# Kernel optimization log

Measured on AMD Instinct MI355X. Metric: run time of the kernel, lower is better.

The kernel has to match this reference:

```python
import jax, jax.numpy as jnp
import numpy as np

NUM_HEADS = 16
EMBD_DIM = 1024


def setup_inputs() -> dict:
    key = jax.random.key(0)
    k_x, k_q, k_k, k_v, k_o = jax.random.split(key, 5)
    BS, SL, ED = 4, 2048, EMBD_DIM
    scale = 1.0 / np.sqrt(ED)
    return {
        "x": jax.random.normal(k_x, (BS, SL, ED), dtype=jnp.float32),
        "Wq": jax.random.normal(k_q, (ED, ED), dtype=jnp.float32) * scale,
        "Wk": jax.random.normal(k_k, (ED, ED), dtype=jnp.float32) * scale,
        "Wv": jax.random.normal(k_v, (ED, ED), dtype=jnp.float32) * scale,
        "Wo": jax.random.normal(k_o, (ED, ED), dtype=jnp.float32) * scale,
    }


def reference(x, Wq, Wk, Wv, Wo):
    BS, SL, ED = x.shape
    NH = NUM_HEADS
    HS = ED // NH
    # QKV projections (no bias), split heads -> [B, H, S, Hs]
    q = (x @ Wq).reshape(BS, SL, NH, HS).transpose(0, 2, 1, 3)
    k = (x @ Wk).reshape(BS, SL, NH, HS).transpose(0, 2, 1, 3)
    v = (x @ Wv).reshape(BS, SL, NH, HS).transpose(0, 2, 1, 3)
    # scaled dot-product scores [B, H, S, S]
    scores = jnp.einsum("bhqd,bhkd->bhqk", q, k) / jnp.sqrt(jnp.float32(HS))
    causal = jnp.tril(jnp.ones((SL, SL), dtype=bool))
    scores = jnp.where(causal, scores, jnp.float32(-jnp.inf))
    attn = jax.nn.softmax(scores, axis=-1)
    # attn_dropout with p=0.0 is identity (eval mode)
    out = jnp.einsum("bhqk,bhkd->bhqd", attn, v)
    out = out.transpose(0, 2, 1, 3).reshape(BS, SL, ED)
    # output projection; resid_dropout p=0.0 is identity
    return out @ Wo
```

## Files before the change

kernel.cpp:

```cpp
#include <hip/hip_runtime.h>

typedef unsigned short u16;
typedef unsigned int u32;
typedef __bf16 bf16x8 __attribute__((ext_vector_type(8)));
typedef float f32x4 __attribute__((ext_vector_type(4)));

__device__ __forceinline__ u16 f2bf(float f) {
  union { float f; u32 u; } v; v.f = f;
  u32 r = v.u + 0x7FFFu + ((v.u >> 16) & 1u);
  return (u16)(r >> 16);
}
__device__ __forceinline__ u32 pk2(float a, float b) {
  return (u32)f2bf(a) | ((u32)f2bf(b) << 16);
}

typedef __attribute__((address_space(1))) const void* gvp;
typedef __attribute__((address_space(3))) void* lvp;
__device__ __forceinline__ void gl16(const u16* g, u16* l) {
  __builtin_amdgcn_global_load_lds((gvp)g, (lvp)l, 16, 0, 0);
}

__global__ void probe_kernel(const u16* __restrict__ x, int* __restrict__ mode) {
  if (threadIdx.x == 0 && blockIdx.x == 0) {
    int cnt = 0;
    for (int i = 0; i < 512; ++i) {
      int e = (x[i] >> 7) & 0xFF;
      cnt += (e >= 110 && e <= 134) ? 1 : 0;
    }
    *mode = (cnt >= 410) ? 1 : 0;
  }
}

__global__ __launch_bounds__(256) void cast_x(const void* __restrict__ src,
                                              u16* __restrict__ dst, int n,
                                              const int* __restrict__ mode) {
  int i = (blockIdx.x * 256 + threadIdx.x) * 8;
  if (i >= n) return;
  uint4 out;
  if (*mode == 0) {
    const float* s = (const float*)src + i;
    float4 v0 = *(const float4*)s, v1 = *(const float4*)(s + 4);
    out.x = pk2(v0.x, v0.y); out.y = pk2(v0.z, v0.w);
    out.z = pk2(v1.x, v1.y); out.w = pk2(v1.z, v1.w);
  } else {
    out = *(const uint4*)((const u16*)src + i);
  }
  *(uint4*)(dst + i) = out;
}

__global__ __launch_bounds__(256) void tcast(const void* __restrict__ src,
                                             u16* __restrict__ dst, int srcld,
                                             int dstld, const int* __restrict__ mode) {
  __shared__ __align__(16) u16 T[64 * 72];
  int k0 = blockIdx.x * 64, n0 = blockIdx.y * 64;
  int tid = threadIdx.x;
  bool bf = (*mode != 0);
#pragma unroll
  for (int p = 0; p < 2; ++p) {
    int idx = (tid + p * 256) * 8;
    int r = idx >> 6, c = idx & 63;
    uint4 o;
    if (!bf) {
      const float* s = (const float*)src + (size_t)(k0 + r) * srcld + n0 + c;
      float4 v0 = *(const float4*)s, v1 = *(const float4*)(s + 4);
      o.x = pk2(v0.x, v0.y); o.y = pk2(v0.z, v0.w);
      o.z = pk2(v1.x, v1.y); o.w = pk2(v1.z, v1.w);
    } else {
      o = *(const uint4*)((const u16*)src + (size_t)(k0 + r) * srcld + n0 + c);
    }
    *(uint4*)&T[r * 72 + c] = o;
  }
  __syncthreads();
#pragma unroll
  for (int p = 0; p < 2; ++p) {
    int idx = (tid + p * 256) * 8;
    int n = idx >> 6, kk = idx & 63;
    u16 v[8];
#pragma unroll
    for (int j = 0; j < 8; ++j) v[j] = T[(kk + j) * 72 + n];
    *(uint4*)(dst + (size_t)(n0 + n) * dstld + k0 + kk) = *(uint4*)v;
  }
}

template<int OUTM>
__global__ __launch_bounds__(256) void gemm_m97(
    const u16* __restrict__ A, const u16* __restrict__ Bt,
    u16* __restrict__ Qb, u16* __restrict__ Kb, u16* __restrict__ VTg,
    float* __restrict__ Cf, int M, int N, int K, const int* __restrict__ mode) {
  __shared__ __align__(16) u16 As[128 * 64];
  __shared__ __align__(16) u16 Bs[128 * 64];
  int tid = threadIdx.x, wid = tid >> 6, lane = tid & 63;
  int wm = wid >> 1, wn = wid & 1, l15 = lane & 15, lq = lane >> 4;
  int m0 = blockIdx.x * 128, n0 = blockIdx.y * 128;
  int rs = lane >> 3, cs = (lane & 7) * 8;

  f32x4 acc[4][4] = {};

  for (int k0 = 0; k0 < K; k0 += 64) {
    __syncthreads();
#pragma unroll
    for (int p = 0; p < 4; ++p) {
      int r = wid * 32 + p * 8;
      gl16(A  + (size_t)(m0 + r + rs) * K + k0 + cs, &As[r * 64]);
      gl16(Bt + (size_t)(n0 + r + rs) * K + k0 + cs, &Bs[r * 64]);
    }
    __syncthreads();
#pragma unroll
    for (int kk = 0; kk < 64; kk += 32) {
      bf16x8 af[4], bfr[4];
#pragma unroll
      for (int x = 0; x < 4; ++x)
        af[x] = *(const bf16x8*)&As[(wm * 64 + x * 16 + l15) * 64 + kk + lq * 8];
#pragma unroll
      for (int x = 0; x < 4; ++x)
        bfr[x] = *(const bf16x8*)&Bs[(wn * 64 + x * 16 + l15) * 64 + kk + lq * 8];
#pragma unroll
      for (int mf = 0; mf < 4; ++mf)
#pragma unroll
        for (int nf = 0; nf < 4; ++nf)
          acc[mf][nf] = __builtin_amdgcn_mfma_f32_16x16x32_bf16(
              af[mf], bfr[nf], acc[mf][nf], 0, 0, 0);
    }
  }

  if (OUTM == 0) {
#pragma unroll
    for (int mf = 0; mf < 4; ++mf)
#pragma unroll
      for (int nf = 0; nf < 4; ++nf) {
        int col = n0 + wn * 64 + nf * 16 + l15;
        int row0 = m0 + wm * 64 + mf * 16 + lq * 4;
        if (col < 1024) {
#pragma unroll
          for (int i = 0; i < 4; ++i)
            Qb[(size_t)(row0 + i) * 1024 + col] = f2bf(acc[mf][nf][i]);
        } else if (col < 2048) {
#pragma unroll
          for (int i = 0; i < 4; ++i)
            Kb[(size_t)(row0 + i) * 1024 + col - 1024] = f2bf(acc[mf][nf][i]);
        } else {
          int np = col - 2048, h = np >> 6, d = np & 63;
          int b = row0 >> 11, s0 = row0 & 2047;
          uint2 w;
          w.x = pk2(acc[mf][nf][0], acc[mf][nf][1]);
          w.y = pk2(acc[mf][nf][2], acc[mf][nf][3]);
          *(uint2*)&VTg[((size_t)(b * 16 + h) * 64 + d) * 2048 + s0] = w;
        }
      }
  } else {
    bool f32out = (*mode == 0);
#pragma unroll
    for (int mf = 0; mf < 4; ++mf)
#pragma unroll
      for (int nf = 0; nf < 4; ++nf) {
        int col = n0 + wn * 64 + nf * 16 + l15;
#pragma unroll
        for (int i = 0; i < 4; ++i) {
          int row = m0 + wm * 64 + mf * 16 + lq * 4 + i;
          float v = acc[mf][nf][i];
          if (f32out) Cf[(size_t)row * N + col] = v;
          else        Qb[(size_t)row * N + col] = f2bf(v);
        }
      }
  }
}

__global__ __launch_bounds__(256) void attn_kernel(
    const u16* __restrict__ Qb, const u16* __restrict__ Kb,
    const u16* __restrict__ VT, u16* __restrict__ O) {
  constexpr int LDP = 136;
  __shared__ __align__(16) u16 Ps[4][32 * LDP];
  int pairi = blockIdx.x, h = blockIdx.y, b = blockIdx.z;
  int tid = threadIdx.x, wid = tid >> 6, lane = tid & 63;
  int l15 = lane & 15, lq = lane >> 4;
  u16* ps = &Ps[wid][0];

  const size_t qoff = (size_t)b * 2048 * 1024 + h * 64;
  const u16* Qp = Qb + qoff;
  const u16* Kp = Kb + qoff;
  const u16* Vp = VT + ((size_t)(b * 16 + h) << 17);
  u16* Op = O + qoff;

  int qts[2] = {pairi, 15 - pairi};
  for (int qi = 0; qi < 2; ++qi) {
    int qt = qts[qi];
    int q0 = qt * 128;
    bf16x8 qf[2][2];
#pragma unroll
    for (int mf = 0; mf < 2; ++mf)
#pragma unroll
      for (int kf = 0; kf < 2; ++kf)
        qf[mf][kf] = *(const bf16x8*)(Qp + (size_t)(q0 + wid * 32 + mf * 16 + l15) * 1024 +
                                      kf * 32 + lq * 8);
    float m_i[2][4], l_i[2][4];
#pragma unroll
    for (int mf = 0; mf < 2; ++mf)
#pragma unroll
      for (int i = 0; i < 4; ++i) { m_i[mf][i] = -1e30f; l_i[mf][i] = 0.f; }
    f32x4 o_acc[2][4] = {};

    for (int t = 0; t <= qt; ++t) {
      int k0 = t * 128;
      f32x4 s[2][8] = {};
#pragma unroll
      for (int kf = 0; kf < 2; ++kf)
#pragma unroll
        for (int nf = 0; nf < 8; ++nf) {
          bf16x8 kfr = *(const bf16x8*)(Kp + (size_t)(k0 + nf * 16 + l15) * 1024 +
                                        kf * 32 + lq * 8);
#pragma unroll
          for (int mf = 0; mf < 2; ++mf)
            s[mf][nf] = __builtin_amdgcn_mfma_f32_16x16x32_bf16(
                qf[mf][kf], kfr, s[mf][nf], 0, 0, 0);
        }
      if (t == qt) {
#pragma unroll
        for (int mf = 0; mf < 2; ++mf)
#pragma unroll
          for (int nf = 0; nf < 8; ++nf) {
            int gk = nf * 16 + l15;
#pragma unroll
            for (int i = 0; i < 4; ++i) {
              int gq = wid * 32 + mf * 16 + lq * 4 + i;
              float v = s[mf][nf][i] * 0.125f;
              s[mf][nf][i] = (gk <= gq) ? v : -1e30f;
            }
          }
      } else {
#pragma unroll
        for (int mf = 0; mf < 2; ++mf)
#pragma unroll
          for (int nf = 0; nf < 8; ++nf)
#pragma unroll
            for (int i = 0; i < 4; ++i) s[mf][nf][i] *= 0.125f;
      }
      float tmax[2][4];
#pragma unroll
      for (int mf = 0; mf < 2; ++mf)
#pragma unroll
        for (int i = 0; i < 4; ++i) {
          float m = -1e30f;
#pragma unroll
          for (int nf = 0; nf < 8; ++nf) m = fmaxf(m, s[mf][nf][i]);
          tmax[mf][i] = m;
        }
#pragma unroll
      for (int msk = 1; msk <= 8; msk <<= 1)
#pragma unroll
        for (int mf = 0; mf < 2; ++mf)
#pragma unroll
          for (int i = 0; i < 4; ++i)
            tmax[mf][i] = fmaxf(tmax[mf][i], __shfl_xor(tmax[mf][i], msk, 64));
      float alpha[2][4], psum[2][4];
#pragma unroll
      for (int mf = 0; mf < 2; ++mf)
#pragma unroll
        for (int i = 0; i < 4; ++i) {
          float mn = fmaxf(m_i[mf][i], tmax[mf][i]);
          alpha[mf][i] = __expf(m_i[mf][i] - mn);
          m_i[mf][i] = mn;
          psum[mf][i] = 0.f;
        }
#pragma unroll
      for (int mf = 0; mf < 2; ++mf)
#pragma unroll
        for (int nf = 0; nf < 8; ++nf)
#pragma unroll
          for (int i = 0; i < 4; ++i) {
            float p = __expf(s[mf][nf][i] - m_i[mf][i]);
            psum[mf][i] += p;
            ps[(mf * 16 + lq * 4 + i) * LDP + nf * 16 + l15] = f2bf(p);
          }
#pragma unroll
      for (int msk = 1; msk <= 8; msk <<= 1)
#pragma unroll
        for (int mf = 0; mf < 2; ++mf)
#pragma unroll
          for (int i = 0; i < 4; ++i) psum[mf][i] += __shfl_xor(psum[mf][i], msk, 64);
#pragma unroll
      for (int mf = 0; mf < 2; ++mf)
#pragma unroll
        for (int i = 0; i < 4; ++i) l_i[mf][i] = l_i[mf][i] * alpha[mf][i] + psum[mf][i];
#pragma unroll
      for (int mf = 0; mf < 2; ++mf)
#pragma unroll
        for (int nf = 0; nf < 4; ++nf)
#pragma unroll
          for (int i = 0; i < 4; ++i) o_acc[mf][nf][i] *= alpha[mf][i];
#pragma unroll
      for (int kf4 = 0; kf4 < 4; ++kf4) {
        bf16x8 pa0 = *(const bf16x8*)&ps[(l15) * LDP + kf4 * 32 + lq * 8];
        bf16x8 pa1 = *(const bf16x8*)&ps[(16 + l15) * LDP + kf4 * 32 + lq * 8];
#pragma unroll
        for (int nf = 0; nf < 4; ++nf) {
          bf16x8 vb = *(const bf16x8*)(Vp + (size_t)(nf * 16 + l15) * 2048 +
                                       k0 + kf4 * 32 + lq * 8);
          o_acc[0][nf] = __builtin_amdgcn_mfma_f32_16x16x32_bf16(pa0, vb, o_acc[0][nf], 0, 0, 0);
          o_acc[1][nf] = __builtin_amdgcn_mfma_f32_16x16x32_bf16(pa1, vb, o_acc[1][nf], 0, 0, 0);
        }
      }
    }
    float rinv[2][4];
#pragma unroll
    for (int mf = 0; mf < 2; ++mf)
#pragma unroll
      for (int i = 0; i < 4; ++i) rinv[mf][i] = 1.0f / l_i[mf][i];
#pragma unroll
    for (int mf = 0; mf < 2; ++mf)
#pragma unroll
      for (int nf = 0; nf < 4; ++nf)
#pragma unroll
        for (int i = 0; i < 4; ++i) {
          int row = q0 + wid * 32 + mf * 16 + lq * 4 + i;
          Op[(size_t)row * 1024 + nf * 16 + l15] = f2bf(o_acc[mf][nf][i] * rinv[mf][i]);
        }
  }
}

extern "C" void kernel_launch(void* const* d_in, const int* in_sizes, int n_in,
                              void* d_out, int out_size, void* d_ws, size_t ws_size,
                              hipStream_t stream) {
  (void)in_sizes; (void)n_in; (void)out_size; (void)ws_size;
  const void* x  = d_in[0];
  const void* Wq = d_in[1];
  const void* Wk = d_in[2];
  const void* Wv = d_in[3];
  const void* Wo = d_in[4];
  const int SL = 2048, ED = 1024;
  const int M = 4 * SL;

  char* ws = (char*)d_ws;
  u16* x_bf  = (u16*)(ws + 0);
  u16* wT    = (u16*)(ws + 16777216);
  u16* wo_T  = (u16*)(ws + 23068672);
  u16* Qb    = (u16*)(ws + 25165824);
  u16* Kb    = (u16*)(ws + 41943040);
  u16* VTg   = (u16*)(ws + 58720256);
  u16* attnb = x_bf;
  int* mode  = (int*)(ws + 75497472);

  probe_kernel<<<1, 64, 0, stream>>>((const u16*)x, mode);

  cast_x<<<(M * ED / 8) / 256, 256, 0, stream>>>(x, x_bf, M * ED, mode);
  tcast<<<dim3(16, 16), 256, 0, stream>>>(Wq, wT + 0,           ED, ED, mode);
  tcast<<<dim3(16, 16), 256, 0, stream>>>(Wk, wT + 1024 * 1024, ED, ED, mode);
  tcast<<<dim3(16, 16), 256, 0, stream>>>(Wv, wT + 2048 * 1024, ED, ED, mode);
  tcast<<<dim3(16, 16), 256, 0, stream>>>(Wo, wo_T,             ED, ED, mode);

  gemm_m97<0><<<dim3(M / 128, (3 * ED) / 128), 256, 0, stream>>>(
      x_bf, wT, Qb, Kb, VTg, nullptr, M, 3 * ED, ED, mode);

  attn_kernel<<<dim3(8, 16, 4), 256, 0, stream>>>(Qb, Kb, VTg, attnb);

  gemm_m97<1><<<dim3(M / 128, ED / 128), 256, 0, stream>>>(
      attnb, wo_T, (u16*)d_out, nullptr, nullptr, (float*)d_out, M, ED, ED, mode);
}
```

Before: 417.3 us.

## Reschedule attention per XCD, use exp2 softmax with MFMA row sums, swizzle GEMM tiles

The GEMM kernel now remaps workgroup IDs so that consecutive tiles go to the same XCD, aiming for better L2 reuse. The attention kernel now launches one workgroup per query tile (1024 total) in longest-first order. Workgroups that share a (batch, head) are grouped onto the same XCD, so their K/V reads can hit a shared L2. Softmax now uses exp2 with the 1/sqrt(d)·log2e scale folded into an FMA, and skips the rescale when no row max grows. Row sums come from an MFMA against a vector of ones instead of shuffles, which adds extra MFMA work per tile.

Result: slower. 497.4 us (+19.2%).

```diff
diff --git a/kernel.cpp b/kernel.cpp
--- a/kernel.cpp
+++ b/kernel.cpp
@@ -91,7 +91,10 @@
   __shared__ __align__(16) u16 Bs[128 * 64];
   int tid = threadIdx.x, wid = tid >> 6, lane = tid & 63;
   int wm = wid >> 1, wn = wid & 1, l15 = lane & 15, lq = lane >> 4;
-  int m0 = blockIdx.x * 128, n0 = blockIdx.y * 128;
+  int nwg = gridDim.x * gridDim.y;
+  int id = blockIdx.y * gridDim.x + blockIdx.x;
+  int swz = (id & 7) * (nwg >> 3) + (id >> 3);
+  int m0 = (swz % gridDim.x) * 128, n0 = (swz / gridDim.x) * 128;
   int rs = lane >> 3, cs = (lane & 7) * 8;
 
   f32x4 acc[4][4] = {};
@@ -169,8 +172,13 @@
     const u16* __restrict__ Qb, const u16* __restrict__ Kb,
     const u16* __restrict__ VT, u16* __restrict__ O) {
   constexpr int LDP = 136;
+  constexpr float SC = 0.18033688f;
   __shared__ __align__(16) u16 Ps[4][32 * LDP];
-  int pairi = blockIdx.x, h = blockIdx.y, b = blockIdx.z;
+  int id = blockIdx.x;
+  int xcd = id & 7, slot = id >> 3;
+  int g = (slot >> 4) * 8 + xcd;
+  int qt = 15 - (slot & 15);
+  int h = g & 15, b = g >> 4;
   int tid = threadIdx.x, wid = tid >> 6, lane = tid & 63;
   int l15 = lane & 15, lq = lane >> 4;
   u16* ps = &Ps[wid][0];
@@ -181,140 +189,128 @@
   const u16* Vp = VT + ((size_t)(b * 16 + h) << 17);
   u16* Op = O + qoff;
 
-  int qts[2] = {pairi, 15 - pairi};
-  for (int qi = 0; qi < 2; ++qi) {
-    int qt = qts[qi];
-    int q0 = qt * 128;
-    bf16x8 qf[2][2];
+  bf16x8 ones;
+#pragma unroll
+  for (int j = 0; j < 8; ++j) ones[j] = (__bf16)1.0f;
+
+  int q0 = qt * 128;
+  bf16x8 qf[2][2];
+#pragma unroll
+  for (int mf = 0; mf < 2; ++mf)
+#pragma unroll
+    for (int kf = 0; kf < 2; ++kf)
+      qf[mf][kf] = *(const bf16x8*)(Qp + (size_t)(q0 + wid * 32 + mf * 16 + l15) * 1024 +
+                                    kf * 32 + lq * 8);
+  float m_i[2][4];
+#pragma unroll
+  for (int mf = 0; mf < 2; ++mf)
+#pragma unroll
+    for (int i = 0; i < 4; ++i) m_i[mf][i] = -1e30f;
+  f32x4 o_acc[2][4] = {};
+  f32x4 lacc[2] = {};
+
+  for (int t = 0; t <= qt; ++t) {
+    int k0 = t * 128;
+    f32x4 s[2][8] = {};
+#pragma unroll
+    for (int kf = 0; kf < 2; ++kf)
+#pragma unroll
+      for (int nf = 0; nf < 8; ++nf) {
+        bf16x8 kfr = *(const bf16x8*)(Kp + (size_t)(k0 + nf * 16 + l15) * 1024 +
+                                      kf * 32 + lq * 8);
+#pragma unroll
+        for (int mf = 0; mf < 2; ++mf)
+          s[mf][nf] = __builtin_amdgcn_mfma_f32_16x16x32_bf16(
+              qf[mf][kf], kfr, s[mf][nf], 0, 0, 0);
+      }
+    if (t == qt) {
+#pragma unroll
+      for (int mf = 0; mf < 2; ++mf)
+#pragma unroll
+        for (int nf = 0; nf < 8; ++nf) {
+          int gk = nf * 16 + l15;
+#pragma unroll
+          for (int i = 0; i < 4; ++i) {
+            int gq = wid * 32 + mf * 16 + lq * 4 + i;
+            if (gk > gq) s[mf][nf][i] = -1e30f;
+          }
+        }
+    }
+    float tmax[2][4];
 #pragma unroll
     for (int mf = 0; mf < 2; ++mf)
 #pragma unroll
-      for (int kf = 0; kf < 2; ++kf)
-        qf[mf][kf] = *(const bf16x8*)(Qp + (size_t)(q0 + wid * 32 + mf * 16 + l15) * 1024 +
-                                      kf * 32 + lq * 8);
-    float m_i[2][4], l_i[2][4];
+      for (int i = 0; i < 4; ++i) {
+        float m = s[mf][0][i];
+#pragma unroll
+        for (int nf = 1; nf < 8; ++nf) m = fmaxf(m, s[mf][nf][i]);
+        tmax[mf][i] = m;
+      }
+#pragma unroll
+    for (int msk = 1; msk <= 8; msk <<= 1)
+#pragma unroll
+      for (int mf = 0; mf < 2; ++mf)
+#pragma unroll
+        for (int i = 0; i < 4; ++i)
+          tmax[mf][i] = fmaxf(tmax[mf][i], __shfl_xor(tmax[mf][i], msk, 64));
+    float mnew[2][4], d = 0.f;
 #pragma unroll
     for (int mf = 0; mf < 2; ++mf)
 #pragma unroll
-      for (int i = 0; i < 4; ++i) { m_i[mf][i] = -1e30f; l_i[mf][i] = 0.f; }
-    f32x4 o_acc[2][4] = {};
-
-    for (int t = 0; t <= qt; ++t) {
-      int k0 = t * 128;
-      f32x4 s[2][8] = {};
-#pragma unroll
-      for (int kf = 0; kf < 2; ++kf)
-#pragma unroll
-        for (int nf = 0; nf < 8; ++nf) {
-          bf16x8 kfr = *(const bf16x8*)(Kp + (size_t)(k0 + nf * 16 + l15) * 1024 +
-                                        kf * 32 + lq * 8);
-#pragma unroll
-          for (int mf = 0; mf < 2; ++mf)
-            s[mf][nf] = __builtin_amdgcn_mfma_f32_16x16x32_bf16(
-                qf[mf][kf], kfr, s[mf][nf], 0, 0, 0);
-        }
-      if (t == qt) {
-#pragma unroll
-        for (int mf = 0; mf < 2; ++mf)
-#pragma unroll
-          for (int nf = 0; nf < 8; ++nf) {
-            int gk = nf * 16 + l15;
-#pragma unroll
-            for (int i = 0; i < 4; ++i) {
-              int gq = wid * 32 + mf * 16 + lq * 4 + i;
-              float v = s[mf][nf][i] * 0.125f;
-              s[mf][nf][i] = (gk <= gq) ? v : -1e30f;
-            }
-          }
-      } else {
-#pragma unroll
-        for (int mf = 0; mf < 2; ++mf)
-#pragma unroll
-          for (int nf = 0; nf < 8; ++nf)
-#pragma unroll
-            for (int i = 0; i < 4; ++i) s[mf][nf][i] *= 0.125f;
-      }
-      float tmax[2][4];
+      for (int i = 0; i < 4; ++i) {
+        mnew[mf][i] = fmaxf(m_i[mf][i], tmax[mf][i] * SC);
+        d = fmaxf(d, mnew[mf][i] - m_i[mf][i]);
+      }
+    if (__any(d > 0.f)) {
 #pragma unroll
       for (int mf = 0; mf < 2; ++mf)
 #pragma unroll
         for (int i = 0; i < 4; ++i) {
-          float m = -1e30f;
-#pragma unroll
-          for (int nf = 0; nf < 8; ++nf) m = fmaxf(m, s[mf][nf][i]);
-          tmax[mf][i] = m;
-        }
-#pragma unroll
-      for (int msk = 1; msk <= 8; msk <<= 1)
-#pragma unroll
-        for (int mf = 0; mf < 2; ++mf)
-#pragma unroll
-          for (int i = 0; i < 4; ++i)
-            tmax[mf][i] = fmaxf(tmax[mf][i], __shfl_xor(tmax[mf][i], msk, 64));
-      float alpha[2][4], psum[2][4];
-#pragma unroll
-      for (int mf = 0; mf < 2; ++mf)
+          float a = __builtin_amdgcn_exp2f(m_i[mf][i] - mnew[mf][i]);
+          m_i[mf][i] = mnew[mf][i];
+#pragma unroll
+          for (int nf = 0; nf < 4; ++nf) o_acc[mf][nf][i] *= a;
+          lacc[mf][i] *= a;
+        }
+    }
+#pragma unroll
+    for (int mf = 0; mf < 2; ++mf)
+#pragma unroll
+      for (int nf = 0; nf < 8; ++nf)
 #pragma unroll
         for (int i = 0; i < 4; ++i) {
-          float mn = fmaxf(m_i[mf][i], tmax[mf][i]);
-          alpha[mf][i] = __expf(m_i[mf][i] - mn);
-          m_i[mf][i] = mn;
-          psum[mf][i] = 0.f;
-        }
-#pragma unroll
-      for (int mf = 0; mf < 2; ++mf)
-#pragma unroll
-        for (int nf = 0; nf < 8; ++nf)
-#pragma unroll
-          for (int i = 0; i < 4; ++i) {
-            float p = __expf(s[mf][nf][i] - m_i[mf][i]);
-            psum[mf][i] += p;
-            ps[(mf * 16 + lq * 4 + i) * LDP + nf * 16 + l15] = f2bf(p);
-          }
-#pragma unroll
-      for (int msk = 1; msk <= 8; msk <<= 1)
-#pragma unroll
-        for (int mf = 0; mf < 2; ++mf)
-#pragma unroll
-          for (int i = 0; i < 4; ++i) psum[mf][i] += __shfl_xor(psum[mf][i], msk, 64);
-#pragma unroll
-      for (int mf = 0; mf < 2; ++mf)
-#pragma unroll
-        for (int i = 0; i < 4; ++i) l_i[mf][i] = l_i[mf][i] * alpha[mf][i] + psum[mf][i];
-#pragma unroll
-      for (int mf = 0; mf < 2; ++mf)
-#pragma unroll
-        for (int nf = 0; nf < 4; ++nf)
-#pragma unroll
-          for (int i = 0; i < 4; ++i) o_acc[mf][nf][i] *= alpha[mf][i];
-#pragma unroll
-      for (int kf4 = 0; kf4 < 4; ++kf4) {
-        bf16x8 pa0 = *(const bf16x8*)&ps[(l15) * LDP + kf4 * 32 + lq * 8];
-        bf16x8 pa1 = *(const bf16x8*)&ps[(16 + l15) * LDP + kf4 * 32 + lq * 8];
-#pragma unroll
-        for (int nf = 0; nf < 4; ++nf) {
-          bf16x8 vb = *(const bf16x8*)(Vp + (size_t)(nf * 16 + l15) * 2048 +
-                                       k0 + kf4 * 32 + lq * 8);
-          o_acc[0][nf] = __builtin_amdgcn_mfma_f32_16x16x32_bf16(pa0, vb, o_acc[0][nf], 0, 0, 0);
-          o_acc[1][nf] = __builtin_amdgcn_mfma_f32_16x16x32_bf16(pa1, vb, o_acc[1][nf], 0, 0, 0);
-        }
-      }
-    }
-    float rinv[2][4];
-#pragma unroll
-    for (int mf = 0; mf < 2; ++mf)
-#pragma unroll
-      for (int i = 0; i < 4; ++i) rinv[mf][i] = 1.0f / l_i[mf][i];
-#pragma unroll
-    for (int mf = 0; mf < 2; ++mf)
-#pragma unroll
-      for (int nf = 0; nf < 4; ++nf)
-#pragma unroll
-        for (int i = 0; i < 4; ++i) {
-          int row = q0 + wid * 32 + mf * 16 + lq * 4 + i;
-          Op[(size_t)row * 1024 + nf * 16 + l15] = f2bf(o_acc[mf][nf][i] * rinv[mf][i]);
-        }
-  }
+          float p = __builtin_amdgcn_exp2f(fmaf(s[mf][nf][i], SC, -m_i[mf][i]));
+          ps[(mf * 16 + lq * 4 + i) * LDP + nf * 16 + l15] = f2bf(p);
+        }
+#pragma unroll
+    for (int kf4 = 0; kf4 < 4; ++kf4) {
+      bf16x8 pa0 = *(const bf16x8*)&ps[(l15) * LDP + kf4 * 32 + lq * 8];
+      bf16x8 pa1 = *(const bf16x8*)&ps[(16 + l15) * LDP + kf4 * 32 + lq * 8];
+      lacc[0] = __builtin_amdgcn_mfma_f32_16x16x32_bf16(pa0, ones, lacc[0], 0, 0, 0);
+      lacc[1] = __builtin_amdgcn_mfma_f32_16x16x32_bf16(pa1, ones, lacc[1], 0, 0, 0);
+#pragma unroll
+      for (int nf = 0; nf < 4; ++nf) {
+        bf16x8 vb = *(const bf16x8*)(Vp + (size_t)(nf * 16 + l15) * 2048 +
+                                     k0 + kf4 * 32 + lq * 8);
+        o_acc[0][nf] = __builtin_amdgcn_mfma_f32_16x16x32_bf16(pa0, vb, o_acc[0][nf], 0, 0, 0);
+        o_acc[1][nf] = __builtin_amdgcn_mfma_f32_16x16x32_bf16(pa1, vb, o_acc[1][nf], 0, 0, 0);
+      }
+    }
+  }
+  float rinv[2][4];
+#pragma unroll
+  for (int mf = 0; mf < 2; ++mf)
+#pragma unroll
+    for (int i = 0; i < 4; ++i) rinv[mf][i] = 1.0f / lacc[mf][i];
+#pragma unroll
+  for (int mf = 0; mf < 2; ++mf)
+#pragma unroll
+    for (int nf = 0; nf < 4; ++nf)
+#pragma unroll
+      for (int i = 0; i < 4; ++i) {
+        int row = q0 + wid * 32 + mf * 16 + lq * 4 + i;
+        Op[(size_t)row * 1024 + nf * 16 + l15] = f2bf(o_acc[mf][nf][i] * rinv[mf][i]);
+      }
 }
 
 extern "C" void kernel_launch(void* const* d_in, const int* in_sizes, int n_in,
@@ -350,7 +346,7 @@
   gemm_m97<0><<<dim3(M / 128, (3 * ED) / 128), 256, 0, stream>>>(
       x_bf, wT, Qb, Kb, VTg, nullptr, M, 3 * ED, ED, mode);
 
-  attn_kernel<<<dim3(8, 16, 4), 256, 0, stream>>>(Qb, Kb, VTg, attnb);
+  attn_kernel<<<dim3(1024), 256, 0, stream>>>(Qb, Kb, VTg, attnb);
 
   gemm_m97<1><<<dim3(M / 128, ED / 128), 256, 0, stream>>>(
       attnb, wo_T, (u16*)d_out, nullptr, nullptr, (float*)d_out, M, ED, ED, mode);
```
